# Kernel tuning notes

Hardware: AMD Instinct MI355X
Metric: run time of the kernel (lower is better)

## Reference

```python
import jax, jax.numpy as jnp
import numpy as np

B, N, E, H, TOP_K = 2, 2048, 1024, 16, 64
Dh = E // H


def _linear_init(k, fan_in, shape):
    bound = 1.0 / np.sqrt(fan_in)
    return jax.random.uniform(k, shape, jnp.float32, -bound, bound)


def setup_inputs() -> dict:
    key = jax.random.key(0)
    ks = jax.random.split(key, 11)
    return {
        "query": jax.random.normal(ks[0], (B, N, E), jnp.float32),
        "key": jax.random.normal(ks[1], (B, N, E), jnp.float32),
        "value": jax.random.normal(ks[2], (B, N, E), jnp.float32),
        "Wq": _linear_init(ks[3], E, (E, E)),
        "bq": _linear_init(ks[4], E, (E,)),
        "Wk": _linear_init(ks[5], E, (E, E)),
        "bk": _linear_init(ks[6], E, (E,)),
        "Wv": _linear_init(ks[7], E, (E, E)),
        "bv": _linear_init(ks[8], E, (E,)),
        "Wo": _linear_init(ks[9], E, (E, E)),
        "bo": _linear_init(ks[10], E, (E,)),
    }


def _split_heads(x):
    # (B, N, E) -> (B*H, N, Dh)
    return x.reshape(B, N, H, Dh).transpose(0, 2, 1, 3).reshape(B * H, N, Dh)


def _merge_heads(x):
    # (B*H, N, Dh) -> (B, N, E)
    return x.reshape(B, H, N, Dh).transpose(0, 2, 1, 3).reshape(B, N, E)


def _topk_attention(q, k, v, top_k):
    # q,k,v: (BH, N, Dh). Faithful to _classical_efficient_attention:
    # scores scaled by sqrt(last dim of Q) == sqrt(Dh).
    scores = jnp.einsum("bqd,bkd->bqk", q, k) / jnp.sqrt(jnp.float32(q.shape[-1]))
    top_scores, top_idx = jax.lax.top_k(scores, min(top_k, scores.shape[-1]))
    w = jax.nn.softmax(top_scores, axis=-1)  # (BH, Nq, K)
    # gather V rows: (BH, 1, Nk, Dh) indexed along axis 2 -> (BH, Nq, K, Dh)
    vals = jnp.take_along_axis(v[:, None, :, :], top_idx[..., None], axis=2)
    return jnp.einsum("bqk,bqkd->bqd", w, vals)


def reference(query, key, value, Wq, bq, Wk, bk, Wv, bv, Wo, bo):
    q = _split_heads(query @ Wq.T + bq)
    k = _split_heads(key @ Wk.T + bk)
    v = _split_heads(value @ Wv.T + bv)
    out = _topk_attention(q, k, v, TOP_K)
    return _merge_heads(out) @ Wo.T + bo
```

## Files before the change

kernel.cpp:

```cpp
#include <hip/hip_runtime.h>
#include <stdint.h>
#include <math.h>

#define Bk 2
#define Nk 2048
#define Ek 1024
#define Hk 16
#define DHk 64
#define BLENDW 5e-5
#define PRECAND 96
#define CANDCAP 128

using short8 = __attribute__((ext_vector_type(8))) short;
using f32x4  = __attribute__((ext_vector_type(4))) float;

__device__ __forceinline__ unsigned short bf16rne(float f) {
    const unsigned u = __float_as_uint(f);
    return (unsigned short)((u + 0x7FFFu + ((u >> 16) & 1u)) >> 16);
}

__global__ __launch_bounds__(256) void cvt_split(
    const float* __restrict__ in, unsigned short* __restrict__ oh,
    unsigned short* __restrict__ ol)
{
    const int i = blockIdx.x * 256 + threadIdx.x;
    const float4 a = ((const float4*)in)[i * 2];
    const float4 b = ((const float4*)in)[i * 2 + 1];
    float x[8] = {a.x, a.y, a.z, a.w, b.x, b.y, b.z, b.w};
    unsigned short hs[8], ls[8];
#pragma unroll
    for (int j = 0; j < 8; ++j) {
        hs[j] = bf16rne(x[j]);
        const float hf = __uint_as_float((unsigned)hs[j] << 16);
        ls[j] = bf16rne(x[j] - hf);
    }
    uint4 ho, lo;
    ho.x = hs[0] | ((unsigned)hs[1] << 16); ho.y = hs[2] | ((unsigned)hs[3] << 16);
    ho.z = hs[4] | ((unsigned)hs[5] << 16); ho.w = hs[6] | ((unsigned)hs[7] << 16);
    lo.x = ls[0] | ((unsigned)ls[1] << 16); lo.y = ls[2] | ((unsigned)ls[3] << 16);
    lo.z = ls[4] | ((unsigned)ls[5] << 16); lo.w = ls[6] | ((unsigned)ls[7] << 16);
    ((uint4*)oh)[i] = ho;
    ((uint4*)ol)[i] = lo;
}

template<int MODE>
__global__ __launch_bounds__(512, 4) void gemm_mfma(
    const unsigned short* __restrict__ Xh, const unsigned short* __restrict__ Xl,
    const unsigned short* __restrict__ Wh, const unsigned short* __restrict__ Wl,
    const float* __restrict__ bias, float* __restrict__ out,
    unsigned short* __restrict__ obf)
{
    __shared__ unsigned short Ah[128][40], Al[128][40];
    __shared__ unsigned short Bh[64][40],  Bl[64][40];

    const int tid  = threadIdx.x;
    const int lane = tid & 63;
    const int wv   = tid >> 6;
    const int n16  = lane & 15;
    const int quad = lane >> 4;
    const int mBase = blockIdx.y * 128;
    const int nBase = blockIdx.x * 64;

    f32x4 acc[4];
#pragma unroll
    for (int j = 0; j < 4; ++j) acc[j] = (f32x4){0.f, 0.f, 0.f, 0.f};

    const int arow = tid >> 2, aoff = (tid & 3) * 8;
    const int brow = tid >> 3, boff = (tid & 7) * 4;
    const size_t aIdx = (size_t)(mBase + arow) * Ek + aoff;
    const size_t bIdx = (size_t)(nBase + brow) * Ek + boff;

    for (int kt = 0; kt < Ek; kt += 32) {
        const uint4 ah0 = *(const uint4*)(Xh + aIdx + kt);
        const uint4 al0 = *(const uint4*)(Xl + aIdx + kt);
        const uint2 bh0 = *(const uint2*)(Wh + bIdx + kt);
        const uint2 bl0 = *(const uint2*)(Wl + bIdx + kt);
        __syncthreads();
        *(uint4*)&Ah[arow][aoff] = ah0;
        *(uint4*)&Al[arow][aoff] = al0;
        *(uint2*)&Bh[brow][boff] = bh0;
        *(uint2*)&Bl[brow][boff] = bl0;
        __syncthreads();

        const short8 fa_h = *(const short8*)&Ah[wv*16 + n16][quad*8];
        const short8 fa_l = *(const short8*)&Al[wv*16 + n16][quad*8];
#pragma unroll
        for (int ct = 0; ct < 4; ++ct) {
            const short8 fb_h = *(const short8*)&Bh[ct*16 + n16][quad*8];
            const short8 fb_l = *(const short8*)&Bl[ct*16 + n16][quad*8];
            acc[ct] = __builtin_amdgcn_mfma_f32_16x16x32_bf16(fa_h, fb_h, acc[ct], 0, 0, 0);
            acc[ct] = __builtin_amdgcn_mfma_f32_16x16x32_bf16(fa_h, fb_l, acc[ct], 0, 0, 0);
            acc[ct] = __builtin_amdgcn_mfma_f32_16x16x32_bf16(fa_l, fb_h, acc[ct], 0, 0, 0);
        }
    }

#pragma unroll
    for (int ct = 0; ct < 4; ++ct) {
        const int c  = nBase + ct*16 + n16;
        const float bv = bias[c];
#pragma unroll
        for (int reg = 0; reg < 4; ++reg) {
            const int m = mBase + wv*16 + quad*4 + reg;
            const float o = acc[ct][reg] + bv;
            size_t dst;
            if (MODE == 0) {
                dst = (size_t)m * Ek + c;
            } else {
                const int bb = m >> 11, nn = m & 2047;
                const int hh = c >> 6,  dd = c & 63;
                dst = (((size_t)(bb*Hk + hh) * Nk) + nn) * DHk + dd;
            }
            out[dst] = o;
            if (MODE == 1 && obf) obf[dst] = bf16rne(o);
        }
    }
}

__device__ __forceinline__ unsigned fkey(float s) {
    const unsigned b = __float_as_uint(s);
    return (b & 0x80000000u) ? ~b : (b | 0x80000000u);
}
__device__ __forceinline__ unsigned long long dkey(double s) {
    unsigned long long b = (unsigned long long)__double_as_longlong(s);
    return (b & 0x8000000000000000ull) ? ~b : (b | 0x8000000000000000ull);
}
__device__ __forceinline__ double dinv(unsigned long long u) {
    const unsigned long long b =
        (u & 0x8000000000000000ull) ? (u & 0x7fffffffffffffffull) : ~u;
    return __longlong_as_double((long long)b);
}

__device__ __forceinline__ int dpp_wsum_i32(int x) {
#define STEP(C) x += __builtin_amdgcn_update_dpp(0, x, C, 0xf, 0xf, true);
    STEP(0x111) STEP(0x112) STEP(0x114) STEP(0x118) STEP(0x142) STEP(0x143)
#undef STEP
    return __builtin_amdgcn_readlane(x, 63);
}
__device__ __forceinline__ float dpp_wsum_f32(float x) {
#define STEP(C) { const int t_ = __builtin_amdgcn_update_dpp(0, __float_as_int(x), C, 0xf, 0xf, true); \
                  x += __int_as_float(t_); }
    STEP(0x111) STEP(0x112) STEP(0x114) STEP(0x118) STEP(0x142) STEP(0x143)
#undef STEP
    return __int_as_float(__builtin_amdgcn_readlane(__float_as_int(x), 63));
}
__device__ __forceinline__ float dpp_wmax_f32(float x) {
#define STEP(C) { const int t_ = __builtin_amdgcn_update_dpp(__float_as_int(x), __float_as_int(x), C, 0xf, 0xf, false); \
                  x = fmaxf(x, __int_as_float(t_)); }
    STEP(0x111) STEP(0x112) STEP(0x114) STEP(0x118) STEP(0x142) STEP(0x143)
#undef STEP
    return __int_as_float(__builtin_amdgcn_readlane(__float_as_int(x), 63));
}
__device__ __forceinline__ unsigned dpp_wmin_u32(unsigned x) {
#define STEP(C) { const unsigned t_ = (unsigned)__builtin_amdgcn_update_dpp((int)x, (int)x, C, 0xf, 0xf, false); \
                  x = x < t_ ? x : t_; }
    STEP(0x111) STEP(0x112) STEP(0x114) STEP(0x118) STEP(0x142) STEP(0x143)
#undef STEP
    return (unsigned)__builtin_amdgcn_readlane((int)x, 63);
}
__device__ __forceinline__ unsigned dpp_wmax_u32(unsigned x) {
#define STEP(C) { const unsigned t_ = (unsigned)__builtin_amdgcn_update_dpp((int)x, (int)x, C, 0xf, 0xf, false); \
                  x = x > t_ ? x : t_; }
    STEP(0x111) STEP(0x112) STEP(0x114) STEP(0x118) STEP(0x142) STEP(0x143)
#undef STEP
    return (unsigned)__builtin_amdgcn_readlane((int)x, 63);
}

__device__ __forceinline__ void proc_row(
    const int lane, const int lrow,
    unsigned s0, unsigned s1, unsigned s2, unsigned s3,
    unsigned s4, unsigned s5, unsigned s6, unsigned s7,
    unsigned s8, unsigned s9, unsigned s10, unsigned s11,
    unsigned s12, unsigned s13, unsigned s14, unsigned s15,
    const float* __restrict__ Kb, const float (*qsf)[68],
    unsigned long long (*ck)[CANDCAP], unsigned (*ci)[CANDCAP],
    unsigned long long (*wvi)[64], unsigned (*eq_idx)[64],
    int& i65_out, float& lam_out)
{
    const unsigned long long lmask = (1ull << lane) - 1ull;

    const unsigned q0 = s0 << 16,  q1 = s1 << 16,  q2 = s2 << 16,  q3 = s3 << 16;
    const unsigned q4 = s4 << 16,  q5 = s5 << 16,  q6 = s6 << 16,  q7 = s7 << 16;
    const unsigned q8 = s8 << 16,  q9 = s9 << 16,  q10 = s10 << 16, q11 = s11 << 16;
    const unsigned q12 = s12 << 16, q13 = s13 << 16, q14 = s14 << 16, q15 = s15 << 16;

    unsigned m1 = 0u, m2 = 0u;
#define T2(V) { const unsigned t_ = (V) < m1 ? (V) : m1; \
                m1 = m1 > (V) ? m1 : (V);  m2 = m2 > t_ ? m2 : t_; }
    T2(s0)  T2(s1)  T2(s2)  T2(s3)  T2(s4)  T2(s5)  T2(s6)  T2(s7)
    T2(s8)  T2(s9)  T2(s10) T2(s11) T2(s12) T2(s13) T2(s14) T2(s15)
    T2(q0)  T2(q1)  T2(q2)  T2(q3)  T2(q4)  T2(q5)  T2(q6)  T2(q7)
    T2(q8)  T2(q9)  T2(q10) T2(q11) T2(q12) T2(q13) T2(q14) T2(q15)
#undef T2
    unsigned lo16 = dpp_wmin_u32(m2) >> 16;
    unsigned hi16 = dpp_wmax_u32(m1) >> 16;

    while (lo16 < hi16) {
        const unsigned mid = lo16 + ((hi16 - lo16) >> 1) + 1u;
        const unsigned M = mid << 16;
        int c0 = 0, c1 = 0, c2 = 0, c3 = 0;
        c0 += (s0  >= M); c0 += (q0  >= M); c0 += (s1  >= M); c0 += (q1  >= M);
        c0 += (s2  >= M); c0 += (q2  >= M); c0 += (s3  >= M); c0 += (q3  >= M);
        c1 += (s4  >= M); c1 += (q4  >= M); c1 += (s5  >= M); c1 += (q5  >= M);
        c1 += (s6  >= M); c1 += (q6  >= M); c1 += (s7  >= M); c1 += (q7  >= M);
        c2 += (s8  >= M); c2 += (q8  >= M); c2 += (s9  >= M); c2 += (q9  >= M);
        c2 += (s10 >= M); c2 += (q10 >= M); c2 += (s11 >= M); c2 += (q11 >= M);
        c3 += (s12 >= M); c3 += (q12 >= M); c3 += (s13 >= M); c3 += (q13 >= M);
        c3 += (s14 >= M); c3 += (q14 >= M); c3 += (s15 >= M); c3 += (q15 >= M);
        const int c = dpp_wsum_i32((c0 + c1) + (c2 + c3));
        if (c >= PRECAND) {
            lo16 = mid;
            if (c <= CANDCAP) break;
        } else hi16 = mid - 1u;
    }
    const unsigned THsh = lo16 << 16;

    int nc = 0;
#define COLH(IDX, PRED) { \
        const bool g = (PRED); \
        const unsigned long long m = __ballot(g); \
        if (g) { \
            const int pos = nc + __popcll(m & lmask); \
            if (pos < CANDCAP) \
                ci[lrow][pos] = (unsigned)((((IDX) >> 3) * 512) + (((IDX) & 7) * 64) + lane); \
        } \
        nc += __popcll(m); }
#define COLW(W, S, Q) COLH(2*(W), (Q) >= THsh) COLH(2*(W)+1, (S) >= THsh)
    COLW(0, s0, q0)    COLW(1, s1, q1)    COLW(2, s2, q2)    COLW(3, s3, q3)
    COLW(4, s4, q4)    COLW(5, s5, q5)    COLW(6, s6, q6)    COLW(7, s7, q7)
    COLW(8, s8, q8)    COLW(9, s9, q9)    COLW(10, s10, q10) COLW(11, s11, q11)
    COLW(12, s12, q12) COLW(13, s13, q13) COLW(14, s14, q14) COLW(15, s15, q15)
#undef COLW
#undef COLH
    if (nc > CANDCAP) nc = CANDCAP;

    const int c8 = lane >> 3, d8 = lane & 7;
    const float* qrow = &qsf[lrow][d8 * 8];
    const double qd0 = (double)qrow[0], qd1 = (double)qrow[1];
    const double qd2 = (double)qrow[2], qd3 = (double)qrow[3];
    const double qd4 = (double)qrow[4], qd5 = (double)qrow[5];
    const double qd6 = (double)qrow[6], qd7 = (double)qrow[7];
    const int nb = (nc + 7) >> 3;
    for (int b = 0; b < nb; ++b) {
        const int s  = b * 8 + c8;
        const int s2 = s < nc ? s : nc - 1;
        const unsigned cidx = ci[lrow][s2];
        const unsigned kb32 = (cidx << 6) + (unsigned)(d8 * 8);
        const float2 kv0 = *(const float2*)(Kb + kb32);
        const float2 kv1 = *(const float2*)(Kb + kb32 + 2);
        const float2 kv2 = *(const float2*)(Kb + kb32 + 4);
        const float2 kv3 = *(const float2*)(Kb + kb32 + 6);
        double acc = 0.0;
        acc = fma(qd0, (double)kv0.x, acc);
        acc = fma(qd1, (double)kv0.y, acc);
        acc = fma(qd2, (double)kv1.x, acc);
        acc = fma(qd3, (double)kv1.y, acc);
        acc = fma(qd4, (double)kv2.x, acc);
        acc = fma(qd5, (double)kv2.y, acc);
        acc = fma(qd6, (double)kv3.x, acc);
        acc = fma(qd7, (double)kv3.y, acc);
        acc += __shfl_xor(acc, 1);
        acc += __shfl_xor(acc, 2);
        acc += __shfl_xor(acc, 4);
        if (d8 == 0 && s < nc) ck[lrow][s] = dkey(acc * 0.125);
    }

    const unsigned long long k0 = (lane      < nc) ? ck[lrow][lane]      : 0ull;
    const unsigned long long k1 = (lane + 64 < nc) ? ck[lrow][lane + 64] : 0ull;
    const unsigned idx0 = ci[lrow][lane];
    const unsigned idx1 = ci[lrow][(lane + 64) & (CANDCAP - 1)];
    const unsigned kh0 = (unsigned)(k0 >> 32), kh1 = (unsigned)(k1 >> 32);
    const unsigned kl0 = (unsigned)k0,         kl1 = (unsigned)k1;

    unsigned H;
    {
        const unsigned i0 = (k0 != 0ull) ? kh0 : 0xFFFFFFFFu;
        const unsigned i1 = (k1 != 0ull) ? kh1 : 0xFFFFFFFFu;
        unsigned lo = dpp_wmin_u32(i0 < i1 ? i0 : i1);
        unsigned hi = dpp_wmax_u32(kh0 > kh1 ? kh0 : kh1);
        bool done = false;
        while (lo < hi) {
            const unsigned mid = lo + ((hi - lo) >> 1) + 1u;
            const int c = __popcll(__ballot(kh0 >= mid))
                        + __popcll(__ballot(kh1 >= mid));
            if (c == 64) {
                const unsigned v0 = (kh0 >= mid) ? kh0 : 0xFFFFFFFFu;
                const unsigned v1 = (kh1 >= mid) ? kh1 : 0xFFFFFFFFu;
                H = dpp_wmin_u32(v0 < v1 ? v0 : v1);
                done = true; break;
            }
            if (c >= 64) lo = mid; else hi = mid - 1u;
        }
        if (!done) H = lo;
    }
    const int cGtHi = __popcll(__ballot(kh0 > H))
                    + __popcll(__ballot(kh1 > H));
    const int need1 = 64 - cGtHi;

    const bool e0v = (kh0 == H) && (k0 != 0ull);
    const bool e1v = (kh1 == H) && (k1 != 0ull);
    const int cEq = __popcll(__ballot(e0v)) + __popcll(__ballot(e1v));
    unsigned Tlo;
    if (need1 == cEq) {
        const unsigned v0 = e0v ? kl0 : 0xFFFFFFFFu;
        const unsigned v1 = e1v ? kl1 : 0xFFFFFFFFu;
        Tlo = dpp_wmin_u32(v0 < v1 ? v0 : v1);
    } else if (need1 == 1) {
        const unsigned v0 = e0v ? kl0 : 0u;
        const unsigned v1 = e1v ? kl1 : 0u;
        Tlo = dpp_wmax_u32(v0 > v1 ? v0 : v1);
    } else {
        unsigned lo = 0u, hi = 0xFFFFFFFFu;
        bool done = false;
        while (lo < hi) {
            const unsigned mid = lo + ((hi - lo) >> 1) + 1u;
            const int c = __popcll(__ballot(e0v && kl0 >= mid))
                        + __popcll(__ballot(e1v && kl1 >= mid));
            if (c == need1) {
                const unsigned v0 = (e0v && kl0 >= mid) ? kl0 : 0xFFFFFFFFu;
                const unsigned v1 = (e1v && kl1 >= mid) ? kl1 : 0xFFFFFFFFu;
                Tlo = dpp_wmin_u32(v0 < v1 ? v0 : v1);
                done = true; break;
            }
            if (c >= need1) lo = mid; else hi = mid - 1u;
        }
        if (!done) Tlo = lo;
    }
    const unsigned long long T = ((unsigned long long)H << 32) | Tlo;

    int base = 0;
    {
        const bool g0 = k0 > T;
        unsigned long long m = __ballot(g0);
        if (g0) {
            const int pos = base + __popcll(m & lmask);
            wvi[lrow][pos] = ((unsigned long long)__float_as_uint((float)dinv(k0)) << 32)
                           | (unsigned long long)idx0;
        }
        base += __popcll(m);
        const bool g1 = k1 > T;
        m = __ballot(g1);
        if (g1) {
            const int pos = base + __popcll(m & lmask);
            wvi[lrow][pos] = ((unsigned long long)__float_as_uint((float)dinv(k1)) << 32)
                           | (unsigned long long)idx1;
        }
        base += __popcll(m);
    }

    int ne = 0;
    {
        const bool e0 = k0 == T;
        unsigned long long m = __ballot(e0);
        if (e0) {
            const int pos = ne + __popcll(m & lmask);
            if (pos < 64) eq_idx[lrow][pos] = idx0;
        }
        ne += __popcll(m);
        const bool e1 = k1 == T;
        m = __ballot(e1);
        if (e1) {
            const int pos = ne + __popcll(m & lmask);
            if (pos < 64) eq_idx[lrow][pos] = idx1;
        }
        ne += __popcll(m);
    }
    if (ne > 64) ne = 64;

    const int   need = 64 - base;
    const float tvf  = (float)dinv(T);
    if (lane < need) {
        unsigned my = 0u;
        for (int j = 0; j < ne; ++j) {
            const unsigned v = eq_idx[lrow][j];
            int rank = 0;
            for (int j2 = 0; j2 < ne; ++j2) rank += (eq_idx[lrow][j2] < v) ? 1 : 0;
            if (rank == lane) my = v;
        }
        wvi[lrow][base + lane] = ((unsigned long long)__float_as_uint(tvf) << 32)
                               | (unsigned long long)my;
    }

    unsigned long long m2k = 0ull;
    if (k0 < T && k0 > m2k) m2k = k0;
    if (k1 < T && k1 > m2k) m2k = k1;
#pragma unroll
    for (int off = 32; off > 0; off >>= 1) {
        const unsigned long long o =
            (unsigned long long)__shfl_xor((long long)m2k, off);
        if (o > m2k) m2k = o;
    }
    int i65 = 0;
    {
        unsigned long long mm = __ballot(k0 == m2k && m2k != 0ull);
        if (mm) i65 = __shfl((int)idx0, (int)(__ffsll((long long)mm) - 1));
        else {
            mm = __ballot(k1 == m2k && m2k != 0ull);
            if (mm) i65 = __shfl((int)idx1, (int)(__ffsll((long long)mm) - 1));
        }
    }
    double fr = (dinv(T) - dinv(m2k)) * (1.0 / BLENDW);
    if (fr > 1.0) fr = 1.0;
    i65_out = i65;
    lam_out = (m2k == 0ull) ? 0.f : (float)(0.5 * (1.0 - fr));
}

__global__ __launch_bounds__(1024, 8) void attn_topk_mfma(
    const float* __restrict__ qf, const float* __restrict__ kf,
    const unsigned short* __restrict__ kbf,
    const float* __restrict__ vh, float* __restrict__ outm)
{
    __shared__ __align__(16) char uS[33024];
    float (*sc)[516] = (float(*)[516])uS;
    unsigned long long (*ck)[CANDCAP] = (unsigned long long(*)[CANDCAP])uS;
    unsigned (*ci)[CANDCAP] = (unsigned(*)[CANDCAP])(uS + 16384);

    __shared__ float          qsf[16][68];
    __shared__ unsigned short qbf[16][72];
    __shared__ unsigned long long wvi[16][64];
    __shared__ unsigned eq_idx[16][64];

    const int tid  = threadIdx.x;
    const int lane = tid & 63;
    const int wv   = tid >> 6;

    const int wid  = (blockIdx.x & 7) * 512 + (blockIdx.x >> 3);
    const int slot = wid >> 7;
    const int qt   = wid & 127;
    const int bb   = slot >> 4;
    const int hh   = slot & 15;

    const float*          Qb = qf  + (size_t)slot * Nk * DHk + (size_t)qt * 16 * DHk;
    const float*          Kb = kf  + (size_t)slot * Nk * DHk;
    const unsigned short* KB = kbf + (size_t)slot * Nk * DHk;
    const float*          Vb = vh  + (size_t)slot * Nk * DHk;

    {
        const int r = tid >> 6, d = tid & 63;
        const float qv = Qb[r * DHk + d];
        qsf[r][d] = qv;
        qbf[r][d] = bf16rne(qv);
    }
    __syncthreads();

    const int n16  = lane & 15;
    const int quad = lane >> 4;
    short8 afrag0, afrag1;
    afrag0 = *(const short8*)&qbf[n16][quad * 8];
    afrag1 = *(const short8*)&qbf[n16][32 + quad * 8];

    unsigned p0, p1, p2, p3, p4, p5, p6, p7;
    unsigned p8, p9, p10, p11, p12, p13, p14, p15;
    const int rowD = quad * 4;

#define QK_TILE(CH, T, ACC) { \
    const unsigned short* kp = KB + ((size_t)(CH) * 512 + (wv * 2 + (T)) * 16 + n16) * DHk + quad * 8; \
    const short8 b0_ = *(const short8*)(kp); \
    const short8 b1_ = *(const short8*)(kp + 32); \
    ACC = __builtin_amdgcn_mfma_f32_16x16x32_bf16(afrag0, b0_, ACC, 0, 0, 0); \
    ACC = __builtin_amdgcn_mfma_f32_16x16x32_bf16(afrag1, b1_, ACC, 0, 0, 0); \
}
#define SC_STORE(T, ACC) { \
    const int ccol = (wv * 2 + (T)) * 16 + n16; \
    sc[rowD + 0][ccol] = ACC[0]; sc[rowD + 1][ccol] = ACC[1]; \
    sc[rowD + 2][ccol] = ACC[2]; sc[rowD + 3][ccol] = ACC[3]; \
}
#define PACKW(J, DEST) { \
    const unsigned lo_ = fkey(sc[wv][(2*(J)    ) * 64 + lane]) >> 16; \
    const unsigned hi_ = fkey(sc[wv][(2*(J) + 1) * 64 + lane]) >> 16; \
    DEST = lo_ | (hi_ << 16); \
}
#define DO_CHUNK(CH, D0, D1, D2, D3) { \
    f32x4 ac0 = {0.f,0.f,0.f,0.f}, ac1 = {0.f,0.f,0.f,0.f}; \
    QK_TILE(CH, 0, ac0) QK_TILE(CH, 1, ac1) \
    __syncthreads();                    \
    SC_STORE(0, ac0) SC_STORE(1, ac1) \
    __syncthreads(); \
    PACKW(0, D0) PACKW(1, D1) PACKW(2, D2) PACKW(3, D3) \
}
    DO_CHUNK(0, p0,  p1,  p2,  p3)
    DO_CHUNK(1, p4,  p5,  p6,  p7)
    DO_CHUNK(2, p8,  p9,  p10, p11)
    DO_CHUNK(3, p12, p13, p14, p15)
#undef DO_CHUNK
#undef PACKW
#undef SC_STORE
#undef QK_TILE

    __syncthreads();

    int i65_0; float lam_0;
    proc_row(lane, wv,
             p0, p1, p2, p3, p4, p5, p6, p7,
             p8, p9, p10, p11, p12, p13, p14, p15,
             Kb, qsf, ck, ci, wvi, eq_idx, i65_0, lam_0);

    {
        const unsigned long long e = wvi[wv][lane];
        const float    sv = __uint_as_float((unsigned)(e >> 32));
        const unsigned vi = (unsigned)e;
        const float mx = dpp_wmax_f32(sv);
        const float p  = __expf(sv - mx);
        const float Z  = dpp_wsum_f32(p);
        const float w  = p / Z;
        wvi[wv][lane] = ((unsigned long long)__float_as_uint(w) << 32)
                      | (unsigned long long)vi;

        float acc = 0.f;
#pragma unroll
        for (int j = 0; j < 64; ++j) {
            const unsigned long long ej = wvi[wv][j];
            const float wj = __uint_as_float((unsigned)(ej >> 32));
            const unsigned ij = (unsigned)ej;
            acc = fmaf(wj, Vb[(ij << 6) + (unsigned)lane], acc);
        }
        {
            const unsigned long long e63 = wvi[wv][63];
            const float    wT  = __uint_as_float((unsigned)(e63 >> 32));
            const unsigned i64 = (unsigned)e63;
            acc += wT * lam_0 *
                   (Vb[((unsigned)i65_0 << 6) + (unsigned)lane]
                  - Vb[(i64 << 6) + (unsigned)lane]);
        }
        const int gq = qt * 16 + wv;
        outm[((size_t)bb * Nk + gq) * Ek + hh * DHk + lane] = acc;
    }
}

extern "C" void kernel_launch(void* const* d_in, const int* in_sizes, int n_in,
                              void* d_out, int out_size, void* d_ws, size_t ws_size,
                              hipStream_t stream)
{
    const float* query = (const float*)d_in[0];
    const float* key   = (const float*)d_in[1];
    const float* value = (const float*)d_in[2];
    const float* Wq    = (const float*)d_in[3];
    const float* bq    = (const float*)d_in[4];
    const float* Wk    = (const float*)d_in[5];
    const float* bk    = (const float*)d_in[6];
    const float* Wv    = (const float*)d_in[7];
    const float* bv    = (const float*)d_in[8];
    const float* Wo    = (const float*)d_in[9];
    const float* bo    = (const float*)d_in[10];
    float* out = (float*)d_out;
    (void)in_sizes; (void)n_in; (void)out_size; (void)ws_size;

    const size_t seg  = (size_t)(Bk * Hk) * Nk * DHk;
    const size_t wseg = (size_t)Ek * Ek;
    float* qfp = (float*)d_ws;
    float* kfp = qfp + seg;
    float* vws = kfp + seg;
    float* aws = vws + seg;
    unsigned short* kbf = (unsigned short*)(aws + seg);
    unsigned short* xh  = kbf + seg;
    unsigned short* xl  = xh + seg;
    unsigned short* wh  = xl + seg;
    unsigned short* wl  = wh + wseg;

    const dim3 blk(256);
    const dim3 blkG(512);
    const dim3 gG(16, 32);
    const int  gX = (int)(seg  / 2048);
    const int  gW = (int)(wseg / 2048);

    hipLaunchKernelGGL(cvt_split, dim3(gX), blk, 0, stream, query, xh, xl);
    hipLaunchKernelGGL(cvt_split, dim3(gW), blk, 0, stream, Wq, wh, wl);
    hipLaunchKernelGGL((gemm_mfma<1>), gG, blkG, 0, stream, xh, xl, wh, wl, bq, qfp, (unsigned short*)nullptr);
    hipLaunchKernelGGL(cvt_split, dim3(gX), blk, 0, stream, key, xh, xl);
    hipLaunchKernelGGL(cvt_split, dim3(gW), blk, 0, stream, Wk, wh, wl);
    hipLaunchKernelGGL((gemm_mfma<1>), gG, blkG, 0, stream, xh, xl, wh, wl, bk, kfp, kbf);
    hipLaunchKernelGGL(cvt_split, dim3(gX), blk, 0, stream, value, xh, xl);
    hipLaunchKernelGGL(cvt_split, dim3(gW), blk, 0, stream, Wv, wh, wl);
    hipLaunchKernelGGL((gemm_mfma<1>), gG, blkG, 0, stream, xh, xl, wh, wl, bv, vws, (unsigned short*)nullptr);
    hipLaunchKernelGGL(attn_topk_mfma, dim3(32 * 128), dim3(1024), 0, stream,
                       qfp, kfp, kbf, vws, aws);
    hipLaunchKernelGGL(cvt_split, dim3(gX), blk, 0, stream, aws, xh, xl);
    hipLaunchKernelGGL(cvt_split, dim3(gW), blk, 0, stream, Wo, wh, wl);
    hipLaunchKernelGGL((gemm_mfma<0>), gG, blkG, 0, stream, xh, xl, wh, wl, bo, out, (unsigned short*)nullptr);
}
```

Baseline: 601.3 us.

## Give each GEMM wave two M-tiles, use prefix-scan candidate compaction

```diff
diff --git a/kernel.cpp b/kernel.cpp
--- a/kernel.cpp
+++ b/kernel.cpp
@@ -44,7 +44,7 @@
 }
 
 template<int MODE>
-__global__ __launch_bounds__(512, 4) void gemm_mfma(
+__global__ __launch_bounds__(256, 4) void gemm_mfma(
     const unsigned short* __restrict__ Xh, const unsigned short* __restrict__ Xl,
     const unsigned short* __restrict__ Wh, const unsigned short* __restrict__ Wl,
     const float* __restrict__ bias, float* __restrict__ out,
@@ -61,47 +61,60 @@
     const int mBase = blockIdx.y * 128;
     const int nBase = blockIdx.x * 64;
 
-    f32x4 acc[4];
-#pragma unroll
-    for (int j = 0; j < 4; ++j) acc[j] = (f32x4){0.f, 0.f, 0.f, 0.f};
-
-    const int arow = tid >> 2, aoff = (tid & 3) * 8;
-    const int brow = tid >> 3, boff = (tid & 7) * 4;
+    f32x4 acc[2][4];
+#pragma unroll
+    for (int i = 0; i < 2; ++i)
+#pragma unroll
+        for (int j = 0; j < 4; ++j) acc[i][j] = (f32x4){0.f, 0.f, 0.f, 0.f};
+
+    const int arow = tid >> 1, aoff = (tid & 1) * 16;
+    const int brow = tid >> 2, boff = (tid & 3) * 8;
     const size_t aIdx = (size_t)(mBase + arow) * Ek + aoff;
     const size_t bIdx = (size_t)(nBase + brow) * Ek + boff;
 
     for (int kt = 0; kt < Ek; kt += 32) {
         const uint4 ah0 = *(const uint4*)(Xh + aIdx + kt);
+        const uint4 ah1 = *(const uint4*)(Xh + aIdx + kt + 8);
         const uint4 al0 = *(const uint4*)(Xl + aIdx + kt);
-        const uint2 bh0 = *(const uint2*)(Wh + bIdx + kt);
-        const uint2 bl0 = *(const uint2*)(Wl + bIdx + kt);
+        const uint4 al1 = *(const uint4*)(Xl + aIdx + kt + 8);
+        const uint4 bh0 = *(const uint4*)(Wh + bIdx + kt);
+        const uint4 bl0 = *(const uint4*)(Wl + bIdx + kt);
         __syncthreads();
-        *(uint4*)&Ah[arow][aoff] = ah0;
-        *(uint4*)&Al[arow][aoff] = al0;
-        *(uint2*)&Bh[brow][boff] = bh0;
-        *(uint2*)&Bl[brow][boff] = bl0;
+        *(uint4*)&Ah[arow][aoff]     = ah0;
+        *(uint4*)&Ah[arow][aoff + 8] = ah1;
+        *(uint4*)&Al[arow][aoff]     = al0;
+        *(uint4*)&Al[arow][aoff + 8] = al1;
+        *(uint4*)&Bh[brow][boff]     = bh0;
+        *(uint4*)&Bl[brow][boff]     = bl0;
         __syncthreads();
 
-        const short8 fa_h = *(const short8*)&Ah[wv*16 + n16][quad*8];
-        const short8 fa_l = *(const short8*)&Al[wv*16 + n16][quad*8];
+        const short8 fa_h0 = *(const short8*)&Ah[wv*32 +      n16][quad*8];
+        const short8 fa_l0 = *(const short8*)&Al[wv*32 +      n16][quad*8];
+        const short8 fa_h1 = *(const short8*)&Ah[wv*32 + 16 + n16][quad*8];
+        const short8 fa_l1 = *(const short8*)&Al[wv*32 + 16 + n16][quad*8];
 #pragma unroll
         for (int ct = 0; ct < 4; ++ct) {
             const short8 fb_h = *(const short8*)&Bh[ct*16 + n16][quad*8];
             const short8 fb_l = *(const short8*)&Bl[ct*16 + n16][quad*8];
-            acc[ct] = __builtin_amdgcn_mfma_f32_16x16x32_bf16(fa_h, fb_h, acc[ct], 0, 0, 0);
-            acc[ct] = __builtin_amdgcn_mfma_f32_16x16x32_bf16(fa_h, fb_l, acc[ct], 0, 0, 0);
-            acc[ct] = __builtin_amdgcn_mfma_f32_16x16x32_bf16(fa_l, fb_h, acc[ct], 0, 0, 0);
-        }
-    }
-
+            acc[0][ct] = __builtin_amdgcn_mfma_f32_16x16x32_bf16(fa_h0, fb_h, acc[0][ct], 0, 0, 0);
+            acc[0][ct] = __builtin_amdgcn_mfma_f32_16x16x32_bf16(fa_h0, fb_l, acc[0][ct], 0, 0, 0);
+            acc[0][ct] = __builtin_amdgcn_mfma_f32_16x16x32_bf16(fa_l0, fb_h, acc[0][ct], 0, 0, 0);
+            acc[1][ct] = __builtin_amdgcn_mfma_f32_16x16x32_bf16(fa_h1, fb_h, acc[1][ct], 0, 0, 0);
+            acc[1][ct] = __builtin_amdgcn_mfma_f32_16x16x32_bf16(fa_h1, fb_l, acc[1][ct], 0, 0, 0);
+            acc[1][ct] = __builtin_amdgcn_mfma_f32_16x16x32_bf16(fa_l1, fb_h, acc[1][ct], 0, 0, 0);
+        }
+    }
+
+#pragma unroll
+    for (int mt = 0; mt < 2; ++mt)
 #pragma unroll
     for (int ct = 0; ct < 4; ++ct) {
         const int c  = nBase + ct*16 + n16;
         const float bv = bias[c];
 #pragma unroll
         for (int reg = 0; reg < 4; ++reg) {
-            const int m = mBase + wv*16 + quad*4 + reg;
-            const float o = acc[ct][reg] + bv;
+            const int m = mBase + wv*32 + mt*16 + quad*4 + reg;
+            const float o = acc[mt][ct][reg] + bv;
             size_t dst;
             if (MODE == 0) {
                 dst = (size_t)m * Ek + c;
@@ -163,6 +176,15 @@
     STEP(0x111) STEP(0x112) STEP(0x114) STEP(0x118) STEP(0x142) STEP(0x143)
 #undef STEP
     return (unsigned)__builtin_amdgcn_readlane((int)x, 63);
+}
+__device__ __forceinline__ int dpp_wprefix_incl_i32(int x) {
+    x += __builtin_amdgcn_update_dpp(0, x, 0x111, 0xf, 0xf, true);
+    x += __builtin_amdgcn_update_dpp(0, x, 0x112, 0xf, 0xf, true);
+    x += __builtin_amdgcn_update_dpp(0, x, 0x114, 0xf, 0xf, true);
+    x += __builtin_amdgcn_update_dpp(0, x, 0x118, 0xf, 0xf, true);
+    x += __builtin_amdgcn_update_dpp(0, x, 0x142, 0xa, 0xf, true);
+    x += __builtin_amdgcn_update_dpp(0, x, 0x143, 0xc, 0xf, true);
+    return x;
 }
 
 __device__ __forceinline__ void proc_row(
@@ -214,24 +236,31 @@
     }
     const unsigned THsh = lo16 << 16;
 
-    int nc = 0;
-#define COLH(IDX, PRED) { \
-        const bool g = (PRED); \
-        const unsigned long long m = __ballot(g); \
-        if (g) { \
-            const int pos = nc + __popcll(m & lmask); \
+    int cnt = 0;
+#define CC(S, Q) { cnt += ((Q) >= THsh); cnt += ((S) >= THsh); }
+    CC(s0, q0)    CC(s1, q1)    CC(s2, q2)    CC(s3, q3)
+    CC(s4, q4)    CC(s5, q5)    CC(s6, q6)    CC(s7, q7)
+    CC(s8, q8)    CC(s9, q9)    CC(s10, q10)  CC(s11, q11)
+    CC(s12, q12)  CC(s13, q13)  CC(s14, q14)  CC(s15, q15)
+#undef CC
+    const int incl = dpp_wprefix_incl_i32(cnt);
+    int pos = incl - cnt;
+    int nc = __builtin_amdgcn_readlane(incl, 63);
+    if (nc > CANDCAP) nc = CANDCAP;
+#define CE(W, S, Q) { \
+        if ((Q) >= THsh) { \
             if (pos < CANDCAP) \
-                ci[lrow][pos] = (unsigned)((((IDX) >> 3) * 512) + (((IDX) & 7) * 64) + lane); \
-        } \
-        nc += __popcll(m); }
-#define COLW(W, S, Q) COLH(2*(W), (Q) >= THsh) COLH(2*(W)+1, (S) >= THsh)
-    COLW(0, s0, q0)    COLW(1, s1, q1)    COLW(2, s2, q2)    COLW(3, s3, q3)
-    COLW(4, s4, q4)    COLW(5, s5, q5)    COLW(6, s6, q6)    COLW(7, s7, q7)
-    COLW(8, s8, q8)    COLW(9, s9, q9)    COLW(10, s10, q10) COLW(11, s11, q11)
-    COLW(12, s12, q12) COLW(13, s13, q13) COLW(14, s14, q14) COLW(15, s15, q15)
-#undef COLW
-#undef COLH
-    if (nc > CANDCAP) nc = CANDCAP;
+                ci[lrow][pos] = (unsigned)((((W) >> 2) * 512) + (((W) & 3) * 128) + 2 * lane); \
+            ++pos; } \
+        if ((S) >= THsh) { \
+            if (pos < CANDCAP) \
+                ci[lrow][pos] = (unsigned)((((W) >> 2) * 512) + (((W) & 3) * 128) + 2 * lane + 1); \
+            ++pos; } }
+    CE(0, s0, q0)     CE(1, s1, q1)     CE(2, s2, q2)     CE(3, s3, q3)
+    CE(4, s4, q4)     CE(5, s5, q5)     CE(6, s6, q6)     CE(7, s7, q7)
+    CE(8, s8, q8)     CE(9, s9, q9)     CE(10, s10, q10)  CE(11, s11, q11)
+    CE(12, s12, q12)  CE(13, s13, q13)  CE(14, s14, q14)  CE(15, s15, q15)
+#undef CE
 
     const int c8 = lane >> 3, d8 = lane & 7;
     const float* qrow = &qsf[lrow][d8 * 8];
@@ -332,17 +361,17 @@
         const bool g0 = k0 > T;
         unsigned long long m = __ballot(g0);
         if (g0) {
-            const int pos = base + __popcll(m & lmask);
-            wvi[lrow][pos] = ((unsigned long long)__float_as_uint((float)dinv(k0)) << 32)
-                           | (unsigned long long)idx0;
+            const int pos2 = base + __popcll(m & lmask);
+            wvi[lrow][pos2] = ((unsigned long long)__float_as_uint((float)dinv(k0)) << 32)
+                            | (unsigned long long)idx0;
         }
         base += __popcll(m);
         const bool g1 = k1 > T;
         m = __ballot(g1);
         if (g1) {
-            const int pos = base + __popcll(m & lmask);
-            wvi[lrow][pos] = ((unsigned long long)__float_as_uint((float)dinv(k1)) << 32)
-                           | (unsigned long long)idx1;
+            const int pos2 = base + __popcll(m & lmask);
+            wvi[lrow][pos2] = ((unsigned long long)__float_as_uint((float)dinv(k1)) << 32)
+                            | (unsigned long long)idx1;
         }
         base += __popcll(m);
     }
@@ -352,15 +381,15 @@
         const bool e0 = k0 == T;
         unsigned long long m = __ballot(e0);
         if (e0) {
-            const int pos = ne + __popcll(m & lmask);
-            if (pos < 64) eq_idx[lrow][pos] = idx0;
+            const int pos2 = ne + __popcll(m & lmask);
+            if (pos2 < 64) eq_idx[lrow][pos2] = idx0;
         }
         ne += __popcll(m);
         const bool e1 = k1 == T;
         m = __ballot(e1);
         if (e1) {
-            const int pos = ne + __popcll(m & lmask);
-            if (pos < 64) eq_idx[lrow][pos] = idx1;
+            const int pos2 = ne + __popcll(m & lmask);
+            if (pos2 < 64) eq_idx[lrow][pos2] = idx1;
         }
         ne += __popcll(m);
     }
@@ -465,9 +494,8 @@
     sc[rowD + 2][ccol] = ACC[2]; sc[rowD + 3][ccol] = ACC[3]; \
 }
 #define PACKW(J, DEST) { \
-    const unsigned lo_ = fkey(sc[wv][(2*(J)    ) * 64 + lane]) >> 16; \
-    const unsigned hi_ = fkey(sc[wv][(2*(J) + 1) * 64 + lane]) >> 16; \
-    DEST = lo_ | (hi_ << 16); \
+    const float2 pr_ = *(const float2*)&sc[wv][(J) * 128 + 2 * lane]; \
+    DEST = (fkey(pr_.x) >> 16) | ((fkey(pr_.y) >> 16) << 16); \
 }
 #define DO_CHUNK(CH, D0, D1, D2, D3) { \
     f32x4 ac0 = {0.f,0.f,0.f,0.f}, ac1 = {0.f,0.f,0.f,0.f}; \
@@ -557,23 +585,22 @@
     unsigned short* wl  = wh + wseg;
 
     const dim3 blk(256);
-    const dim3 blkG(512);
     const dim3 gG(16, 32);
     const int  gX = (int)(seg  / 2048);
     const int  gW = (int)(wseg / 2048);
 
     hipLaunchKernelGGL(cvt_split, dim3(gX), blk, 0, stream, query, xh, xl);
     hipLaunchKernelGGL(cvt_split, dim3(gW), blk, 0, stream, Wq, wh, wl);
-    hipLaunchKernelGGL((gemm_mfma<1>), gG, blkG, 0, stream, xh, xl, wh, wl, bq, qfp, (unsigned short*)nullptr);
+    hipLaunchKernelGGL((gemm_mfma<1>), gG, blk, 0, stream, xh, xl, wh, wl, bq, qfp, (unsigned short*)nullptr);
     hipLaunchKernelGGL(cvt_split, dim3(gX), blk, 0, stream, key, xh, xl);
     hipLaunchKernelGGL(cvt_split, dim3(gW), blk, 0, stream, Wk, wh, wl);
-    hipLaunchKernelGGL((gemm_mfma<1>), gG, blkG, 0, stream, xh, xl, wh, wl, bk, kfp, kbf);
+    hipLaunchKernelGGL((gemm_mfma<1>), gG, blk, 0, stream, xh, xl, wh, wl, bk, kfp, kbf);
     hipLaunchKernelGGL(cvt_split, dim3(gX), blk, 0, stream, value, xh, xl);
     hipLaunchKernelGGL(cvt_split, dim3(gW), blk, 0, stream, Wv, wh, wl);
-    hipLaunchKernelGGL((gemm_mfma<1>), gG, blkG, 0, stream, xh, xl, wh, wl, bv, vws, (unsigned short*)nullptr);
+    hipLaunchKernelGGL((gemm_mfma<1>), gG, blk, 0, stream, xh, xl, wh, wl, bv, vws, (unsigned short*)nullptr);
     hipLaunchKernelGGL(attn_topk_mfma, dim3(32 * 128), dim3(1024), 0, stream,
                        qfp, kfp, kbf, vws, aws);
     hipLaunchKernelGGL(cvt_split, dim3(gX), blk, 0, stream, aws, xh, xl);
     hipLaunchKernelGGL(cvt_split, dim3(gW), blk, 0, stream, Wo, wh, wl);
-    hipLaunchKernelGGL((gemm_mfma<0>), gG, blkG, 0, stream, xh, xl, wh, wl, bo, out, (unsigned short*)nullptr);
-}
+    hipLaunchKernelGGL((gemm_mfma<0>), gG, blk, 0, stream, xh, xl, wh, wl, bo, out, (unsigned short*)nullptr);
+}
```

Result: faster. 580.9 us (-3.4%).
